# Optimization experiments

Hardware: AMD Instinct MI355X
Metric: run time of the kernel (lower is better)

The kernel has to match this reference:

```python
import jax, jax.numpy as jnp
import numpy as np

NUM_NEURONS = 8192
INPUT_SIZE = 512
OUTPUT_SIZE = 512
TAU = 10.0
G = 1.5


def setup_inputs() -> dict:
    key = jax.random.key(0)
    k1, k2, k3, k4, k5 = jax.random.split(key, 5)
    inputs = jax.random.normal(k1, (INPUT_SIZE,), dtype=jnp.float32)
    potentials = jax.random.normal(k2, (1, NUM_NEURONS), dtype=jnp.float32)
    # parameters, matching the torch init scales
    W_in = jax.random.normal(k3, (INPUT_SIZE, NUM_NEURONS), dtype=jnp.float32) * 0.1
    synapses = jax.random.normal(k4, (NUM_NEURONS, NUM_NEURONS), dtype=jnp.float32) / np.sqrt(NUM_NEURONS).astype(np.float32)
    W_out = jax.random.normal(k5, (NUM_NEURONS, OUTPUT_SIZE), dtype=jnp.float32) / np.float32(NUM_NEURONS)
    return {"inputs": inputs, "potentials": potentials, "W_in": W_in,
            "synapses": synapses, "W_out": W_out}


def reference(inputs, potentials, W_in, synapses, W_out):
    # input_map: bias-free linear, then unsqueeze to [1, N]
    drive = (inputs @ W_in)[None, :]                      # [1, N]
    # Neurons: continuous-time leaky integrator (FORCE-style)
    rates = jnp.tanh(potentials)                          # [1, N]
    pot_new = potentials + (-potentials + G * (rates @ synapses) + drive) / TAU
    gen_net = jnp.tanh(pot_new)                           # [1, N]
    # read_out: bias-free linear
    output = gen_net @ W_out                              # [1, output_size]
    return (output, pot_new)
```

## Files before the change

kernel.cpp:

```cpp
#include <hip/hip_runtime.h>
#include <math.h>

#define N_NEU   8192
#define IN_SZ   512
#define OUT_SZ  512
#define N4      (N_NEU / 4)
#define OUT4    (OUT_SZ / 4)
#define KPB     64
#define SYN_TILES (N_NEU / KPB)
#define WIN_TILES (IN_SZ / KPB)
#define TILES     (SYN_TILES + WIN_TILES)
#define K2_KPB  128
#define OTILES  (N_NEU / K2_KPB)
constexpr float TAU_INV = 0.1f;
constexpr float G_GAIN  = 1.5f;

__global__ __launch_bounds__(256)
void accum_kernel(const float* __restrict__ pot,
                  const float* __restrict__ inputs,
                  const float* __restrict__ synapses,
                  const float* __restrict__ W_in,
                  float4* __restrict__ P4,
                  float* __restrict__ out) {
    __shared__ float xs[KPB];
    const int bx = blockIdx.x, by = blockIdx.y;
    const int tid = threadIdx.x;
    const float4* M;
    int k0;
    if (by < SYN_TILES) {
        k0 = by * KPB;
        M  = (const float4*)synapses;
        if (tid < KPB) xs[tid] = G_GAIN * tanhf(pot[k0 + tid]);
    } else {
        k0 = (by - SYN_TILES) * KPB;
        M  = (const float4*)W_in;
        if (tid < KPB) xs[tid] = inputs[k0 + tid];
    }
    if (by == TILES - 1 && tid < 64) out[bx * 64 + tid] = 0.0f;
    __syncthreads();

    const int col4 = bx * 256 + tid;
    const float4* Mp = M + (size_t)k0 * N4 + col4;

    float4 acc = make_float4(0.f, 0.f, 0.f, 0.f);
#pragma unroll 8
    for (int i = 0; i < KPB; ++i) {
        float  s = xs[i];
        float4 m = Mp[(size_t)i * N4];
        acc.x = fmaf(s, m.x, acc.x);
        acc.y = fmaf(s, m.y, acc.y);
        acc.z = fmaf(s, m.z, acc.z);
        acc.w = fmaf(s, m.w, acc.w);
    }
    P4[(size_t)(by * 8 + bx) * 256 + tid] = acc;
}

__global__ __launch_bounds__(128)
void finish_kernel(const float* __restrict__ pot,
                   const float* __restrict__ P,
                   const float* __restrict__ W_out,
                   float* __restrict__ out) {
    const int b = blockIdx.x;
    const int t = threadIdx.x;
    if (b < OTILES) {
        __shared__ float xs[K2_KPB];
        const int k0  = b * K2_KPB;
        const int bx  = k0 >> 10;
        const int off = (k0 & 1023) + t;
        float s = 0.f;
#pragma unroll 8
        for (int by = 0; by < TILES; ++by)
            s += P[(size_t)(by * 8 + bx) * 1024 + off];
        float p  = pot[k0 + t];
        float pn = p + (s - p) * TAU_INV;
        xs[t] = tanhf(pn);
        __syncthreads();

        const float4* Wp = (const float4*)W_out + (size_t)k0 * OUT4 + t;
        float4 acc = make_float4(0.f, 0.f, 0.f, 0.f);
#pragma unroll 8
        for (int i = 0; i < K2_KPB; ++i) {
            float  sx = xs[i];
            float4 m  = Wp[(size_t)i * OUT4];
            acc.x = fmaf(sx, m.x, acc.x);
            acc.y = fmaf(sx, m.y, acc.y);
            acc.z = fmaf(sx, m.z, acc.z);
            acc.w = fmaf(sx, m.w, acc.w);
        }
        float* op = out + (size_t)t * 4;
        atomicAdd(op + 0, acc.x);
        atomicAdd(op + 1, acc.y);
        atomicAdd(op + 2, acc.z);
        atomicAdd(op + 3, acc.w);
    } else {
        const int j   = (b - OTILES) * 128 + t;
        const int bx  = j >> 10;
        const int off = j & 1023;
        float s = 0.f;
#pragma unroll 8
        for (int by = 0; by < TILES; ++by)
            s += P[(size_t)(by * 8 + bx) * 1024 + off];
        float p  = pot[j];
        float pn = p + (s - p) * TAU_INV;
        out[OUT_SZ + j] = pn;
    }
}

extern "C" void kernel_launch(void* const* d_in, const int* in_sizes, int n_in,
                              void* d_out, int out_size, void* d_ws, size_t ws_size,
                              hipStream_t stream) {
    const float* inputs   = (const float*)d_in[0];
    const float* pot      = (const float*)d_in[1];
    const float* W_in     = (const float*)d_in[2];
    const float* synapses = (const float*)d_in[3];
    const float* W_out    = (const float*)d_in[4];

    float* out = (float*)d_out;
    float* P   = (float*)d_ws;

    accum_kernel<<<dim3(8, TILES), dim3(256), 0, stream>>>(
        pot, inputs, synapses, W_in, (float4*)P, out);

    finish_kernel<<<dim3(OTILES + N_NEU / 128), dim3(128), 0, stream>>>(
        pot, P, W_out, out);
}
```

Before: 405.3 us.

## Fold W_in tiles into synapse tiles and halve readout K-chunk

Each accumulation block now processes 64 synapse rows plus 4 W_in rows, so the separate W_in tiles disappear and the partial-sum buffer shrinks from 136 to 128 tiles per column. This cuts the reduction work in the finish kernel and removes the imbalance between synapse and W_in blocks. The finish kernel's readout K-chunk drops from 128 to 64, which doubles the number of readout blocks and atomics while making each block shorter.

```diff
diff --git a/kernel.cpp b/kernel.cpp
--- a/kernel.cpp
+++ b/kernel.cpp
@@ -6,11 +6,10 @@
 #define OUT_SZ  512
 #define N4      (N_NEU / 4)
 #define OUT4    (OUT_SZ / 4)
-#define KPB     64
-#define SYN_TILES (N_NEU / KPB)
-#define WIN_TILES (IN_SZ / KPB)
-#define TILES     (SYN_TILES + WIN_TILES)
-#define K2_KPB  128
+#define KPB_SYN 64
+#define KPB_WIN 4
+#define TILES   (N_NEU / KPB_SYN)
+#define K2_KPB  64
 #define OTILES  (N_NEU / K2_KPB)
 constexpr float TAU_INV = 0.1f;
 constexpr float G_GAIN  = 1.5f;
@@ -22,31 +21,36 @@
                   const float* __restrict__ W_in,
                   float4* __restrict__ P4,
                   float* __restrict__ out) {
-    __shared__ float xs[KPB];
+    __shared__ float xs[KPB_SYN + KPB_WIN];
     const int bx = blockIdx.x, by = blockIdx.y;
     const int tid = threadIdx.x;
-    const float4* M;
-    int k0;
-    if (by < SYN_TILES) {
-        k0 = by * KPB;
-        M  = (const float4*)synapses;
-        if (tid < KPB) xs[tid] = G_GAIN * tanhf(pot[k0 + tid]);
-    } else {
-        k0 = (by - SYN_TILES) * KPB;
-        M  = (const float4*)W_in;
-        if (tid < KPB) xs[tid] = inputs[k0 + tid];
-    }
+    const int ks = by * KPB_SYN;
+    const int kw = by * KPB_WIN;
+    if (tid < KPB_SYN)
+        xs[tid] = G_GAIN * tanhf(pot[ks + tid]);
+    else if (tid < KPB_SYN + KPB_WIN)
+        xs[tid] = inputs[kw + (tid - KPB_SYN)];
     if (by == TILES - 1 && tid < 64) out[bx * 64 + tid] = 0.0f;
     __syncthreads();
 
     const int col4 = bx * 256 + tid;
-    const float4* Mp = M + (size_t)k0 * N4 + col4;
+    const float4* Sp = (const float4*)synapses + (size_t)ks * N4 + col4;
+    const float4* Wp = (const float4*)W_in     + (size_t)kw * N4 + col4;
 
     float4 acc = make_float4(0.f, 0.f, 0.f, 0.f);
 #pragma unroll 8
-    for (int i = 0; i < KPB; ++i) {
+    for (int i = 0; i < KPB_SYN; ++i) {
         float  s = xs[i];
-        float4 m = Mp[(size_t)i * N4];
+        float4 m = Sp[(size_t)i * N4];
+        acc.x = fmaf(s, m.x, acc.x);
+        acc.y = fmaf(s, m.y, acc.y);
+        acc.z = fmaf(s, m.z, acc.z);
+        acc.w = fmaf(s, m.w, acc.w);
+    }
+#pragma unroll
+    for (int i = 0; i < KPB_WIN; ++i) {
+        float  s = xs[KPB_SYN + i];
+        float4 m = Wp[(size_t)i * N4];
         acc.x = fmaf(s, m.x, acc.x);
         acc.y = fmaf(s, m.y, acc.y);
         acc.z = fmaf(s, m.z, acc.z);
@@ -64,16 +68,18 @@
     const int t = threadIdx.x;
     if (b < OTILES) {
         __shared__ float xs[K2_KPB];
-        const int k0  = b * K2_KPB;
-        const int bx  = k0 >> 10;
-        const int off = (k0 & 1023) + t;
-        float s = 0.f;
+        const int k0 = b * K2_KPB;
+        const int bx = k0 >> 10;
+        if (t < K2_KPB) {
+            const int off = (k0 & 1023) + t;
+            float s = 0.f;
 #pragma unroll 8
-        for (int by = 0; by < TILES; ++by)
-            s += P[(size_t)(by * 8 + bx) * 1024 + off];
-        float p  = pot[k0 + t];
-        float pn = p + (s - p) * TAU_INV;
-        xs[t] = tanhf(pn);
+            for (int by = 0; by < TILES; ++by)
+                s += P[(size_t)(by * 8 + bx) * 1024 + off];
+            float p  = pot[k0 + t];
+            float pn = p + (s - p) * TAU_INV;
+            xs[t] = tanhf(pn);
+        }
         __syncthreads();
 
         const float4* Wp = (const float4*)W_out + (size_t)k0 * OUT4 + t;
```

After: 407.6 us. No clear change (+0.6%).
